# Performance work log

Hardware: AMD Instinct MI355X
Metric: run time of the kernel (lower is better)

The kernel has to match this reference:

```python
import jax, jax.numpy as jnp
import numpy as np

D_MODEL = 1024
NHEADS = 16
DIM_K = D_MODEL // NHEADS


def setup_inputs() -> dict:
    key = jax.random.key(0)
    ks = jax.random.split(key, 7)
    B, S = 4, 2048
    scale = 1.0 / np.sqrt(D_MODEL)
    return {
        "Q": jax.random.normal(ks[0], (B, S, D_MODEL), jnp.float32),
        "K": jax.random.normal(ks[1], (B, S, D_MODEL), jnp.float32),
        "V": jax.random.normal(ks[2], (B, S, D_MODEL), jnp.float32),
        "Wq": jax.random.normal(ks[3], (D_MODEL, D_MODEL), jnp.float32) * scale,
        "Wk": jax.random.normal(ks[4], (D_MODEL, D_MODEL), jnp.float32) * scale,
        "Wv": jax.random.normal(ks[5], (D_MODEL, D_MODEL), jnp.float32) * scale,
        "Wo": jax.random.normal(ks[6], (D_MODEL, D_MODEL), jnp.float32) * scale,
    }


def _split(x):
    # [B,S,D] -> [B,H,S,dk]
    B, S, _ = x.shape
    return x.reshape(B, S, NHEADS, DIM_K).transpose(0, 2, 1, 3)


def reference(Q, K, V, Wq, Wk, Wv, Wo):
    # nn.Linear(x) = x @ W.T; weights stored torch-style [out, in]
    q = _split(Q @ Wq.T)  # [B,H,S,dk]
    k = _split(K @ Wk.T)
    v = _split(V @ Wv.T)
    scores = jnp.einsum("bhsd,bhtd->bhst", q, k) / jnp.sqrt(jnp.float32(DIM_K))
    attn = jax.nn.softmax(scores, axis=-1)
    out = jnp.einsum("bhst,bhtd->bhsd", attn, v)  # [B,H,S,dk]
    B, H, S, dk = out.shape
    out = out.transpose(0, 2, 1, 3).reshape(B, S, H * dk)
    return out @ Wo.T
```

## Files before the change

kernel.cpp:

```cpp
#include <hip/hip_runtime.h>
#include <math.h>
#include <stdint.h>

#define D_MODEL 1024
#define NHEADS  16
#define DK      64
#define BATCH   4
#define SEQ     2048
#define MROWS   (BATCH * SEQ)
#define TENS    ((size_t)MROWS * D_MODEL)
#define WELT    ((size_t)D_MODEL * D_MODEL)

typedef __attribute__((ext_vector_type(8))) _Float16 f16x8;
typedef __attribute__((ext_vector_type(4))) float f32x4;
typedef __attribute__((ext_vector_type(8))) unsigned short us8;
typedef __attribute__((ext_vector_type(4))) unsigned short us4;

__device__ __forceinline__ unsigned short f2h(float x) {
    _Float16 h = (_Float16)x;
    return __builtin_bit_cast(unsigned short, h);
}

__device__ __forceinline__ void gld_lds16(const void* g, void* l) {
    __builtin_amdgcn_global_load_lds(
        (__attribute__((address_space(1))) void*)(uintptr_t)(g),
        (__attribute__((address_space(3))) void*)(unsigned)(uintptr_t)(l),
        16, 0, 0);
}

__global__ __launch_bounds__(256)
void convert_kernel(const float* __restrict__ q, const float* __restrict__ k,
                    const float* __restrict__ v, const float* __restrict__ wq,
                    const float* __restrict__ wk, const float* __restrict__ wv,
                    const float* __restrict__ wo, unsigned short* __restrict__ dst)
{
    const int seg = blockIdx.y;
    const float* src;
    size_t n, doff;
    if (seg < 3) {
        src = (seg == 0) ? q : (seg == 1) ? k : v;
        n = TENS; doff = (size_t)seg * TENS;
    } else {
        src = (seg == 3) ? wq : (seg == 4) ? wk : (seg == 5) ? wv : wo;
        n = WELT; doff = 3 * TENS + (size_t)(seg - 3) * WELT;
    }
    size_t i = ((size_t)blockIdx.x * 256 + threadIdx.x) * 4;
    if (i >= n) return;
    float4 f = *(const float4*)(src + i);
    us4 o = { f2h(f.x), f2h(f.y), f2h(f.z), f2h(f.w) };
    *(us4*)(dst + doff + i) = o;
}

template <int OMODE>
__global__ __launch_bounds__(256)
void gemm_f16(const unsigned short* __restrict__ A,
              const unsigned short* __restrict__ B,
              void* __restrict__ C, int M, int N, int K)
{
    __shared__ unsigned short As[128 * 64];
    __shared__ unsigned short Bs[128 * 64];

    const int tid  = threadIdx.x;
    const int wave = tid >> 6;
    const int lane = tid & 63;
    const int g    = lane >> 4;
    const int m15  = lane & 15;
    const int bm   = blockIdx.x * 128;
    const int bn   = blockIdx.y * 128;

    const int srw = lane >> 3;
    const int lc  = (lane & 7) ^ srw;

    const int wr = (wave >> 1) * 64;
    const int wc = (wave & 1) * 64;

    f32x4 acc[4][4];
#pragma unroll
    for (int i = 0; i < 4; ++i)
#pragma unroll
        for (int j = 0; j < 4; ++j) acc[i][j] = (f32x4){0.f, 0.f, 0.f, 0.f};

    for (int k0 = 0; k0 < K; k0 += 64) {
        __syncthreads();
#pragma unroll
        for (int i = 0; i < 4; ++i) {
            const int rb = wave * 32 + i * 8;
            gld_lds16(A + (size_t)(bm + rb + srw) * K + k0 + lc * 8,
                      &As[rb * 64]);
            gld_lds16(B + (size_t)(bn + rb + srw) * K + k0 + lc * 8,
                      &Bs[rb * 64]);
        }
        __syncthreads();

#pragma unroll
        for (int t = 0; t < 2; ++t) {
            f16x8 af[4], bf[4];
#pragma unroll
            for (int i = 0; i < 4; ++i) {
                int row = wr + i * 16 + m15;
                int pc  = (4 * t + g) ^ (row & 7);
                af[i] = *(const f16x8*)&As[row * 64 + pc * 8];
            }
#pragma unroll
            for (int j = 0; j < 4; ++j) {
                int row = wc + j * 16 + m15;
                int pc  = (4 * t + g) ^ (row & 7);
                bf[j] = *(const f16x8*)&Bs[row * 64 + pc * 8];
            }
#pragma unroll
            for (int i = 0; i < 4; ++i)
#pragma unroll
                for (int j = 0; j < 4; ++j)
                    acc[i][j] = __builtin_amdgcn_mfma_f32_16x16x32_f16(
                        af[i], bf[j], acc[i][j], 0, 0, 0);
        }
    }

#pragma unroll
    for (int i = 0; i < 4; ++i) {
        const int gm0 = bm + wr + i * 16 + g * 4;
#pragma unroll
        for (int j = 0; j < 4; ++j) {
            const int gn = bn + wc + j * 16 + m15;
            if (OMODE == 0) {
#pragma unroll
                for (int r = 0; r < 4; ++r)
                    ((float*)C)[(size_t)(gm0 + r) * N + gn] = acc[i][j][r];
            } else if (OMODE == 1) {
#pragma unroll
                for (int r = 0; r < 4; ++r)
                    ((unsigned short*)C)[(size_t)(gm0 + r) * N + gn] = f2h(acc[i][j][r]);
            } else {
                const int b_ = gm0 >> 11, s_ = gm0 & 2047;
                const int h_ = gn >> 6,  d_ = gn & 63;
                us4 o = { f2h(acc[i][j][0]), f2h(acc[i][j][1]),
                          f2h(acc[i][j][2]), f2h(acc[i][j][3]) };
                *(us4*)((unsigned short*)C +
                        (((size_t)(b_ * NHEADS + h_) * DK + d_) << 11) + s_) = o;
            }
        }
    }
}

__global__ __launch_bounds__(256, 4)
void attn_kernel(const unsigned short* __restrict__ qp,
                 const unsigned short* __restrict__ kp,
                 const unsigned short* __restrict__ vt,
                 unsigned short* __restrict__ ao)
{
    __shared__ unsigned short Ks[64 * 64];
    __shared__ unsigned short VTs[64 * 64];
    __shared__ unsigned short Ps[4][32 * 72];

    const int tid = threadIdx.x;
    const int w = tid >> 6, lane = tid & 63;
    const int g = lane >> 4, m15 = lane & 15;
    const int qt = blockIdx.x, h = blockIdx.y, b = blockIdx.z;

    const int q0 = qt * 128 + w * 32;
    const size_t rowbase = (size_t)b * SEQ;

    const int srw = lane >> 3;
    const int lc  = (lane & 7) ^ srw;

    f16x8 qf[2][2];
#pragma unroll
    for (int mi = 0; mi < 2; ++mi)
#pragma unroll
        for (int t = 0; t < 2; ++t) {
            f16x8 v = *(const f16x8*)(qp + (rowbase + q0 + mi * 16 + m15) * D_MODEL
                                      + h * DK + t * 32 + g * 8);
            qf[mi][t] = v * (_Float16)0.125f;
        }

    float mrun[2] = {-INFINITY, -INFINITY};
    float lrun[2] = {0.f, 0.f};

    f32x4 accO[2][4];
#pragma unroll
    for (int mi = 0; mi < 2; ++mi)
#pragma unroll
        for (int i = 0; i < 4; ++i) accO[mi][i] = (f32x4){0.f, 0.f, 0.f, 0.f};

    const unsigned short* kbase = kp + rowbase * D_MODEL + h * DK;
    const unsigned short* vbase = vt + (size_t)(b * NHEADS + h) * DK * SEQ;

    for (int kt = 0; kt < SEQ / 64; ++kt) {
        __syncthreads();
#pragma unroll
        for (int it = 0; it < 2; ++it) {
            const int rb = w * 16 + it * 8;
            gld_lds16(kbase + (size_t)(kt * 64 + rb + srw) * D_MODEL + lc * 8,
                      &Ks[rb * 64]);
            gld_lds16(vbase + (size_t)(rb + srw) * SEQ + kt * 64 + lc * 8,
                      &VTs[rb * 64]);
        }
        __syncthreads();

        f32x4 ST[4][2];
#pragma unroll
        for (int km = 0; km < 4; ++km) {
            const int row = km * 16 + m15;
            f16x8 kf0 = *(const f16x8*)&Ks[row * 64 + ((0 + g) ^ (row & 7)) * 8];
            f16x8 kf1 = *(const f16x8*)&Ks[row * 64 + ((4 + g) ^ (row & 7)) * 8];
#pragma unroll
            for (int mi = 0; mi < 2; ++mi) {
                f32x4 z = (f32x4){0.f, 0.f, 0.f, 0.f};
                z = __builtin_amdgcn_mfma_f32_16x16x32_f16(kf0, qf[mi][0], z, 0, 0, 0);
                z = __builtin_amdgcn_mfma_f32_16x16x32_f16(kf1, qf[mi][1], z, 0, 0, 0);
                ST[km][mi] = z;
            }
        }

        float scl[2];
#pragma unroll
        for (int mi = 0; mi < 2; ++mi) {
            float mx = -INFINITY;
#pragma unroll
            for (int km = 0; km < 4; ++km)
#pragma unroll
                for (int r = 0; r < 4; ++r) mx = fmaxf(mx, ST[km][mi][r]);
            mx = fmaxf(mx, __shfl_xor(mx, 16));
            mx = fmaxf(mx, __shfl_xor(mx, 32));
            float mnew = fmaxf(mrun[mi], mx);
            scl[mi] = __expf(mrun[mi] - mnew);
            mrun[mi] = mnew;
            float rs = 0.f;
#pragma unroll
            for (int km = 0; km < 4; ++km) {
#pragma unroll
                for (int r = 0; r < 4; ++r) {
                    float p = __expf(ST[km][mi][r] - mnew);
                    ST[km][mi][r] = p;
                    rs += p;
                }
                us4 o = { f2h(ST[km][mi][0]), f2h(ST[km][mi][1]),
                          f2h(ST[km][mi][2]), f2h(ST[km][mi][3]) };
                *(us4*)&Ps[w][(mi * 16 + m15) * 72 + km * 16 + g * 4] = o;
            }
            rs += __shfl_xor(rs, 16);
            rs += __shfl_xor(rs, 32);
            lrun[mi] = lrun[mi] * scl[mi] + rs;
        }

        f16x8 pf[2][2];
#pragma unroll
        for (int mi = 0; mi < 2; ++mi) {
            pf[mi][0] = *(const f16x8*)&Ps[w][(mi * 16 + m15) * 72 + g * 8];
            pf[mi][1] = *(const f16x8*)&Ps[w][(mi * 16 + m15) * 72 + 32 + g * 8];
        }

#pragma unroll
        for (int i = 0; i < 4; ++i) {
            const int row = i * 16 + m15;
            f16x8 vf0 = *(const f16x8*)&VTs[row * 64 + ((0 + g) ^ (row & 7)) * 8];
            f16x8 vf1 = *(const f16x8*)&VTs[row * 64 + ((4 + g) ^ (row & 7)) * 8];
#pragma unroll
            for (int mi = 0; mi < 2; ++mi) {
                f32x4 a = accO[mi][i] * scl[mi];
                a = __builtin_amdgcn_mfma_f32_16x16x32_f16(vf0, pf[mi][0], a, 0, 0, 0);
                a = __builtin_amdgcn_mfma_f32_16x16x32_f16(vf1, pf[mi][1], a, 0, 0, 0);
                accO[mi][i] = a;
            }
        }
    }

#pragma unroll
    for (int mi = 0; mi < 2; ++mi) {
        const float li = 1.f / lrun[mi];
        const size_t qg = rowbase + q0 + mi * 16 + m15;
#pragma unroll
        for (int i = 0; i < 4; ++i) {
            us4 o = { f2h(accO[mi][i][0] * li), f2h(accO[mi][i][1] * li),
                      f2h(accO[mi][i][2] * li), f2h(accO[mi][i][3] * li) };
            *(us4*)(ao + qg * D_MODEL + h * DK + i * 16 + g * 4) = o;
        }
    }
}

extern "C" void kernel_launch(void* const* d_in, const int* in_sizes, int n_in,
                              void* d_out, int out_size, void* d_ws, size_t ws_size,
                              hipStream_t stream)
{
    const float* Q  = (const float*)d_in[0];
    const float* K  = (const float*)d_in[1];
    const float* V  = (const float*)d_in[2];
    const float* Wq = (const float*)d_in[3];
    const float* Wk = (const float*)d_in[4];
    const float* Wv = (const float*)d_in[5];
    const float* Wo = (const float*)d_in[6];

    unsigned short* base = (unsigned short*)d_ws;
    unsigned short* qb = base;
    unsigned short* kb = qb + TENS;
    unsigned short* vb = kb + TENS;
    unsigned short* wq = vb + TENS;
    unsigned short* wk = wq + WELT;
    unsigned short* wv = wk + WELT;
    unsigned short* wo = wv + WELT;
    unsigned short* qproj = wo + WELT;
    unsigned short* kproj = qproj + TENS;
    unsigned short* vtw   = kproj + TENS;
    unsigned short* aow   = vtw + TENS;

    convert_kernel<<<dim3(TENS / 1024, 7), 256, 0, stream>>>(Q, K, V, Wq, Wk, Wv, Wo, base);

    gemm_f16<1><<<dim3(MROWS / 128, D_MODEL / 128), 256, 0, stream>>>(
        qb, wq, qproj, MROWS, D_MODEL, D_MODEL);
    gemm_f16<1><<<dim3(MROWS / 128, D_MODEL / 128), 256, 0, stream>>>(
        kb, wk, kproj, MROWS, D_MODEL, D_MODEL);
    gemm_f16<2><<<dim3(MROWS / 128, D_MODEL / 128), 256, 0, stream>>>(
        vb, wv, vtw, MROWS, D_MODEL, D_MODEL);

    attn_kernel<<<dim3(SEQ / 128, NHEADS, BATCH), 256, 0, stream>>>(
        qproj, kproj, vtw, aow);

    gemm_f16<0><<<dim3(MROWS / 128, D_MODEL / 128), 256, 0, stream>>>(
        aow, wo, (float*)d_out, MROWS, D_MODEL, D_MODEL);
}
```

Before: 374.5 us.

## Merge QKV projections into one launch and enlarge attention query tile

Folds the three projection GEMMs into a single launch indexed by blockIdx.z, and turns the templated GEMM into a shared device body with a runtime output mode. The attention kernel now gives each wave 64 query rows instead of 32, so every K/V tile staged in LDS is reused across twice as many queries, and the occupancy hint drops from 4 to 2 blocks. Softmax switches to exp2 with log2(e) folded into the query scale, packs P to fp16 with cvt_pkrtz, and skips rescaling the output accumulator when no running max changed in the wave. The larger tile raises register pressure and halves the number of attention blocks, and round-toward-zero packing slightly changes rounding.

```diff
diff --git a/kernel.cpp b/kernel.cpp
--- a/kernel.cpp
+++ b/kernel.cpp
@@ -12,6 +12,7 @@
 #define WELT    ((size_t)D_MODEL * D_MODEL)
 
 typedef __attribute__((ext_vector_type(8))) _Float16 f16x8;
+typedef __attribute__((ext_vector_type(2))) __fp16 h16x2;
 typedef __attribute__((ext_vector_type(4))) float f32x4;
 typedef __attribute__((ext_vector_type(8))) unsigned short us8;
 typedef __attribute__((ext_vector_type(4))) unsigned short us4;
@@ -20,6 +21,12 @@
     _Float16 h = (_Float16)x;
     return __builtin_bit_cast(unsigned short, h);
 }
+
+#if __has_builtin(__builtin_amdgcn_exp2f)
+__device__ __forceinline__ float fexp2(float x) { return __builtin_amdgcn_exp2f(x); }
+#else
+__device__ __forceinline__ float fexp2(float x) { return exp2f(x); }
+#endif
 
 __device__ __forceinline__ void gld_lds16(const void* g, void* l) {
     __builtin_amdgcn_global_load_lds(
@@ -51,15 +58,12 @@
     *(us4*)(dst + doff + i) = o;
 }
 
-template <int OMODE>
-__global__ __launch_bounds__(256)
-void gemm_f16(const unsigned short* __restrict__ A,
-              const unsigned short* __restrict__ B,
-              void* __restrict__ C, int M, int N, int K)
-{
-    __shared__ unsigned short As[128 * 64];
-    __shared__ unsigned short Bs[128 * 64];
-
+__device__ __forceinline__
+void gemm_body(const unsigned short* __restrict__ A,
+               const unsigned short* __restrict__ B,
+               void* __restrict__ C, int N, int K, int omode,
+               unsigned short* As, unsigned short* Bs)
+{
     const int tid  = threadIdx.x;
     const int wave = tid >> 6;
     const int lane = tid & 63;
@@ -122,11 +126,11 @@
 #pragma unroll
         for (int j = 0; j < 4; ++j) {
             const int gn = bn + wc + j * 16 + m15;
-            if (OMODE == 0) {
+            if (omode == 0) {
 #pragma unroll
                 for (int r = 0; r < 4; ++r)
                     ((float*)C)[(size_t)(gm0 + r) * N + gn] = acc[i][j][r];
-            } else if (OMODE == 1) {
+            } else if (omode == 1) {
 #pragma unroll
                 for (int r = 0; r < 4; ++r)
                     ((unsigned short*)C)[(size_t)(gm0 + r) * N + gn] = f2h(acc[i][j][r]);
@@ -142,7 +146,37 @@
     }
 }
 
-__global__ __launch_bounds__(256, 4)
+__global__ __launch_bounds__(256)
+void proj3_kernel(const unsigned short* __restrict__ qb,
+                  const unsigned short* __restrict__ kb,
+                  const unsigned short* __restrict__ vb,
+                  const unsigned short* __restrict__ wq,
+                  const unsigned short* __restrict__ wk,
+                  const unsigned short* __restrict__ wv,
+                  unsigned short* __restrict__ qproj,
+                  unsigned short* __restrict__ kproj,
+                  unsigned short* __restrict__ vtw)
+{
+    __shared__ unsigned short As[128 * 64];
+    __shared__ unsigned short Bs[128 * 64];
+    const int z = blockIdx.z;
+    const unsigned short* A = (z == 0) ? qb : (z == 1) ? kb : vb;
+    const unsigned short* B = (z == 0) ? wq : (z == 1) ? wk : wv;
+    void* C = (z == 0) ? (void*)qproj : (z == 1) ? (void*)kproj : (void*)vtw;
+    gemm_body(A, B, C, D_MODEL, D_MODEL, (z == 2) ? 2 : 1, As, Bs);
+}
+
+__global__ __launch_bounds__(256)
+void gemm_out_kernel(const unsigned short* __restrict__ A,
+                     const unsigned short* __restrict__ B,
+                     float* __restrict__ C)
+{
+    __shared__ unsigned short As[128 * 64];
+    __shared__ unsigned short Bs[128 * 64];
+    gemm_body(A, B, C, D_MODEL, D_MODEL, 0, As, Bs);
+}
+
+__global__ __launch_bounds__(256, 2)
 void attn_kernel(const unsigned short* __restrict__ qp,
                  const unsigned short* __restrict__ kp,
                  const unsigned short* __restrict__ vt,
@@ -150,35 +184,36 @@
 {
     __shared__ unsigned short Ks[64 * 64];
     __shared__ unsigned short VTs[64 * 64];
-    __shared__ unsigned short Ps[4][32 * 72];
+    __shared__ unsigned short Ps[4][64 * 72];
 
     const int tid = threadIdx.x;
     const int w = tid >> 6, lane = tid & 63;
     const int g = lane >> 4, m15 = lane & 15;
     const int qt = blockIdx.x, h = blockIdx.y, b = blockIdx.z;
 
-    const int q0 = qt * 128 + w * 32;
+    const int q0 = qt * 256 + w * 64;
     const size_t rowbase = (size_t)b * SEQ;
 
     const int srw = lane >> 3;
     const int lc  = (lane & 7) ^ srw;
 
-    f16x8 qf[2][2];
-#pragma unroll
-    for (int mi = 0; mi < 2; ++mi)
+    const _Float16 qscale = (_Float16)(0.125f * 1.4426950408889634f);
+    f16x8 qf[4][2];
+#pragma unroll
+    for (int mi = 0; mi < 4; ++mi)
 #pragma unroll
         for (int t = 0; t < 2; ++t) {
             f16x8 v = *(const f16x8*)(qp + (rowbase + q0 + mi * 16 + m15) * D_MODEL
                                       + h * DK + t * 32 + g * 8);
-            qf[mi][t] = v * (_Float16)0.125f;
-        }
-
-    float mrun[2] = {-INFINITY, -INFINITY};
-    float lrun[2] = {0.f, 0.f};
-
-    f32x4 accO[2][4];
-#pragma unroll
-    for (int mi = 0; mi < 2; ++mi)
+            qf[mi][t] = v * qscale;
+        }
+
+    float mrun[4] = {-INFINITY, -INFINITY, -INFINITY, -INFINITY};
+    float lrun[4] = {0.f, 0.f, 0.f, 0.f};
+
+    f32x4 accO[4][4];
+#pragma unroll
+    for (int mi = 0; mi < 4; ++mi)
 #pragma unroll
         for (int i = 0; i < 4; ++i) accO[mi][i] = (f32x4){0.f, 0.f, 0.f, 0.f};
 
@@ -197,14 +232,14 @@
         }
         __syncthreads();
 
-        f32x4 ST[4][2];
+        f32x4 ST[4][4];
 #pragma unroll
         for (int km = 0; km < 4; ++km) {
             const int row = km * 16 + m15;
             f16x8 kf0 = *(const f16x8*)&Ks[row * 64 + ((0 + g) ^ (row & 7)) * 8];
             f16x8 kf1 = *(const f16x8*)&Ks[row * 64 + ((4 + g) ^ (row & 7)) * 8];
 #pragma unroll
-            for (int mi = 0; mi < 2; ++mi) {
+            for (int mi = 0; mi < 4; ++mi) {
                 f32x4 z = (f32x4){0.f, 0.f, 0.f, 0.f};
                 z = __builtin_amdgcn_mfma_f32_16x16x32_f16(kf0, qf[mi][0], z, 0, 0, 0);
                 z = __builtin_amdgcn_mfma_f32_16x16x32_f16(kf1, qf[mi][1], z, 0, 0, 0);
@@ -212,9 +247,9 @@
             }
         }
 
-        float scl[2];
-#pragma unroll
-        for (int mi = 0; mi < 2; ++mi) {
+        float scl[4];
+#pragma unroll
+        for (int mi = 0; mi < 4; ++mi) {
             float mx = -INFINITY;
 #pragma unroll
             for (int km = 0; km < 4; ++km)
@@ -223,29 +258,38 @@
             mx = fmaxf(mx, __shfl_xor(mx, 16));
             mx = fmaxf(mx, __shfl_xor(mx, 32));
             float mnew = fmaxf(mrun[mi], mx);
-            scl[mi] = __expf(mrun[mi] - mnew);
+            scl[mi] = fexp2(mrun[mi] - mnew);
             mrun[mi] = mnew;
             float rs = 0.f;
 #pragma unroll
             for (int km = 0; km < 4; ++km) {
-#pragma unroll
-                for (int r = 0; r < 4; ++r) {
-                    float p = __expf(ST[km][mi][r] - mnew);
-                    ST[km][mi][r] = p;
-                    rs += p;
-                }
-                us4 o = { f2h(ST[km][mi][0]), f2h(ST[km][mi][1]),
-                          f2h(ST[km][mi][2]), f2h(ST[km][mi][3]) };
-                *(us4*)&Ps[w][(mi * 16 + m15) * 72 + km * 16 + g * 4] = o;
+                float p0 = fexp2(ST[km][mi][0] - mnew);
+                float p1 = fexp2(ST[km][mi][1] - mnew);
+                float p2 = fexp2(ST[km][mi][2] - mnew);
+                float p3 = fexp2(ST[km][mi][3] - mnew);
+                rs += (p0 + p1) + (p2 + p3);
+                h16x2 d0 = __builtin_amdgcn_cvt_pkrtz(p0, p1);
+                h16x2 d1 = __builtin_amdgcn_cvt_pkrtz(p2, p3);
+                uint2 wv = { __builtin_bit_cast(unsigned, d0),
+                             __builtin_bit_cast(unsigned, d1) };
+                *(uint2*)&Ps[w][(mi * 16 + m15) * 72 + km * 16 + g * 4] = wv;
             }
             rs += __shfl_xor(rs, 16);
             rs += __shfl_xor(rs, 32);
             lrun[mi] = lrun[mi] * scl[mi] + rs;
         }
 
-        f16x8 pf[2][2];
-#pragma unroll
-        for (int mi = 0; mi < 2; ++mi) {
+        int chg = (scl[0] < 1.f) | (scl[1] < 1.f) | (scl[2] < 1.f) | (scl[3] < 1.f);
+        if (__any(chg)) {
+#pragma unroll
+            for (int mi = 0; mi < 4; ++mi)
+#pragma unroll
+                for (int i = 0; i < 4; ++i) accO[mi][i] *= scl[mi];
+        }
+
+        f16x8 pf[4][2];
+#pragma unroll
+        for (int mi = 0; mi < 4; ++mi) {
             pf[mi][0] = *(const f16x8*)&Ps[w][(mi * 16 + m15) * 72 + g * 8];
             pf[mi][1] = *(const f16x8*)&Ps[w][(mi * 16 + m15) * 72 + 32 + g * 8];
         }
@@ -256,8 +300,8 @@
             f16x8 vf0 = *(const f16x8*)&VTs[row * 64 + ((0 + g) ^ (row & 7)) * 8];
             f16x8 vf1 = *(const f16x8*)&VTs[row * 64 + ((4 + g) ^ (row & 7)) * 8];
 #pragma unroll
-            for (int mi = 0; mi < 2; ++mi) {
-                f32x4 a = accO[mi][i] * scl[mi];
+            for (int mi = 0; mi < 4; ++mi) {
+                f32x4 a = accO[mi][i];
                 a = __builtin_amdgcn_mfma_f32_16x16x32_f16(vf0, pf[mi][0], a, 0, 0, 0);
                 a = __builtin_amdgcn_mfma_f32_16x16x32_f16(vf1, pf[mi][1], a, 0, 0, 0);
                 accO[mi][i] = a;
@@ -266,7 +310,7 @@
     }
 
 #pragma unroll
-    for (int mi = 0; mi < 2; ++mi) {
+    for (int mi = 0; mi < 4; ++mi) {
         const float li = 1.f / lrun[mi];
         const size_t qg = rowbase + q0 + mi * 16 + m15;
 #pragma unroll
@@ -305,16 +349,12 @@
 
     convert_kernel<<<dim3(TENS / 1024, 7), 256, 0, stream>>>(Q, K, V, Wq, Wk, Wv, Wo, base);
 
-    gemm_f16<1><<<dim3(MROWS / 128, D_MODEL / 128), 256, 0, stream>>>(
-        qb, wq, qproj, MROWS, D_MODEL, D_MODEL);
-    gemm_f16<1><<<dim3(MROWS / 128, D_MODEL / 128), 256, 0, stream>>>(
-        kb, wk, kproj, MROWS, D_MODEL, D_MODEL);
-    gemm_f16<2><<<dim3(MROWS / 128, D_MODEL / 128), 256, 0, stream>>>(
-        vb, wv, vtw, MROWS, D_MODEL, D_MODEL);
-
-    attn_kernel<<<dim3(SEQ / 128, NHEADS, BATCH), 256, 0, stream>>>(
+    proj3_kernel<<<dim3(MROWS / 128, D_MODEL / 128, 3), 256, 0, stream>>>(
+        qb, kb, vb, wq, wk, wv, qproj, kproj, vtw);
+
+    attn_kernel<<<dim3(SEQ / 256, NHEADS, BATCH), 256, 0, stream>>>(
         qproj, kproj, vtw, aow);
 
-    gemm_f16<0><<<dim3(MROWS / 128, D_MODEL / 128), 256, 0, stream>>>(
-        aow, wo, (float*)d_out, MROWS, D_MODEL, D_MODEL);
-}
+    gemm_out_kernel<<<dim3(MROWS / 128, D_MODEL / 128), 256, 0, stream>>>(
+        aow, wo, (float*)d_out);
+}
```

Result: faster. 342.5 us (-8.5%).
